# Kernel tuning notes

Measured on AMD Instinct MI355X. Metric: run time of the kernel, lower is better.

Reference implementation:

```python
import jax, jax.numpy as jnp
import numpy as np

DIM = 1024
H = 16
HD = 64

def setup_inputs() -> dict:
    key = jax.random.key(0)
    ks = jax.random.split(key, 5)
    x = jax.random.normal(ks[0], (2, 2048, DIM), dtype=jnp.float32)
    gamma = jnp.ones((DIM,), jnp.float32)
    beta = jnp.zeros((DIM,), jnp.float32)
    w_qkv = jax.random.normal(ks[1], (DIM, 3 * H * HD), dtype=jnp.float32) * (DIM ** -0.5)
    w_out = jax.random.normal(ks[2], (H * HD, DIM), dtype=jnp.float32) * ((H * HD) ** -0.5)
    b_out = jnp.zeros((DIM,), jnp.float32)
    return {"x": x, "gamma": gamma, "beta": beta, "w_qkv": w_qkv, "w_out": w_out, "b_out": b_out}

def reference(x, gamma, beta, w_qkv, w_out, b_out):
    # LayerNorm (pre-norm)
    mu = jnp.mean(x, axis=-1, keepdims=True)
    var = jnp.var(x, axis=-1, keepdims=True)
    xn = (x - mu) * jax.lax.rsqrt(var + 1e-5) * gamma + beta
    # QKV projection (no bias)
    qkv = xn @ w_qkv  # (b, n, 3*h*hd)
    q, k, v = jnp.split(qkv, 3, axis=-1)
    b, n, _ = x.shape
    split = lambda t: t.reshape(b, n, H, HD).transpose(0, 2, 1, 3)  # b h n d
    q, k, v = split(q), split(k), split(v)
    scale = HD ** -0.5
    scores = jnp.einsum('bhqd,bhkd->bhqk', q, k) * scale
    weights = jax.nn.softmax(scores, axis=-1)
    attn = jnp.einsum('bhqk,bhkd->bhqd', weights, v)  # b h n d
    attn = attn.transpose(0, 2, 1, 3).reshape(b, n, H * HD)
    # output projection (dropout is identity in eval)
    return attn @ w_out + b_out
```

## Files before the change

kernel.cpp:

```cpp
#include <hip/hip_runtime.h>
#include <hip/hip_bf16.h>


typedef _Float16 f16x8 __attribute__((ext_vector_type(8)));
typedef _Float16 f16x4 __attribute__((ext_vector_type(4)));
typedef float    f32x4 __attribute__((ext_vector_type(4)));

#define DIM   1024
#define NH    16
#define HD2   64
#define SEQ   2048
#define ROWS  4096
#define QKVN  3072
#define NT    32

__device__ __forceinline__ void async_copy16(void* lds, const void* gsrc) {
    __builtin_amdgcn_global_load_lds(
        (const __attribute__((address_space(1))) unsigned int*)gsrc,
        (__attribute__((address_space(3))) unsigned int*)lds, 16, 0, 0);
}

__global__ __launch_bounds__(256) void prologue_kernel(
    const float* __restrict__ x, const float* __restrict__ gamma,
    const float* __restrict__ beta, _Float16* __restrict__ xn,
    const float* __restrict__ w_qkv, _Float16* __restrict__ wqkvT,
    const float* __restrict__ w_out, _Float16* __restrict__ woutT) {
    __shared__ float smem[32 * 33];
    const int bid = blockIdx.x;
    const int t = threadIdx.x;
    if (bid < ROWS) {
        const int row = bid;
        const float4 v = reinterpret_cast<const float4*>(x + (size_t)row * DIM)[t];
        float s1 = v.x + v.y + v.z + v.w;
        float s2 = v.x * v.x + v.y * v.y + v.z * v.z + v.w * v.w;
        for (int off = 32; off; off >>= 1) {
            s1 += __shfl_down(s1, off);
            s2 += __shfl_down(s2, off);
        }
        const int wv = t >> 6, lane = t & 63;
        if (lane == 0) { smem[wv * 2] = s1; smem[wv * 2 + 1] = s2; }
        __syncthreads();
        s1 = smem[0] + smem[2] + smem[4] + smem[6];
        s2 = smem[1] + smem[3] + smem[5] + smem[7];
        const float mu = s1 * (1.0f / DIM);
        const float var = s2 * (1.0f / DIM) - mu * mu;
        const float rstd = rsqrtf(var + 1e-5f);
        const float4 g = reinterpret_cast<const float4*>(gamma)[t];
        const float4 bb = reinterpret_cast<const float4*>(beta)[t];
        f16x4 o;
        o[0] = (_Float16)((v.x - mu) * rstd * g.x + bb.x);
        o[1] = (_Float16)((v.y - mu) * rstd * g.y + bb.y);
        o[2] = (_Float16)((v.z - mu) * rstd * g.z + bb.z);
        o[3] = (_Float16)((v.w - mu) * rstd * g.w + bb.w);
        reinterpret_cast<f16x4*>(xn + (size_t)row * DIM)[t] = o;
        return;
    }
    const float* in;
    _Float16* out;
    int C, bx, by;
    if (bid < ROWS + (QKVN / 32) * (DIM / 32)) {
        const int q = bid - ROWS;
        in = w_qkv; out = wqkvT; C = QKVN;
        bx = q % (QKVN / 32); by = q / (QKVN / 32);
    } else {
        const int q = bid - ROWS - (QKVN / 32) * (DIM / 32);
        in = w_out; out = woutT; C = DIM;
        bx = q % (DIM / 32); by = q / (DIM / 32);
    }
    const int R = DIM;
    const int c0 = bx * 32, r0 = by * 32;
    const int tx = t & 31, ty = t >> 5;
    float (*tile)[33] = reinterpret_cast<float(*)[33]>(smem);
#pragma unroll
    for (int i = 0; i < 4; i++)
        tile[ty + i * 8][tx] = in[(size_t)(r0 + ty + i * 8) * C + c0 + tx];
    __syncthreads();
#pragma unroll
    for (int i = 0; i < 4; i++)
        out[(size_t)(c0 + ty + i * 8) * R + r0 + tx] = (_Float16)tile[tx][ty + i * 8];
}

__global__ __launch_bounds__(256) void gemm_qkv_kernel(
    const _Float16* __restrict__ A, const _Float16* __restrict__ Bt,
    _Float16* __restrict__ qk, _Float16* __restrict__ vT) {
    const int K = DIM;
    __shared__ _Float16 Al[3][128 * 32];
    __shared__ _Float16 Bl[3][128 * 32];
    const int t = threadIdx.x, wv = t >> 6, lane = t & 63;
    const int lg = lane >> 4, lr = lane & 15;
    const int wr = wv >> 1, wc = wv & 1;
    const int m0 = blockIdx.y * 128, n0 = blockIdx.x * 128;

    f32x4 acc[4][4] = {};

    const int srow = t >> 2, sk = (t & 3) * 8;
    const _Float16* Ag0 = A + (size_t)(m0 + srow) * K + sk;
    const _Float16* Bg0 = Bt + (size_t)(n0 + srow) * K + sk;

    auto STAGE = [&](int buf, int k0) {
        _Float16* Alw = &Al[buf][wv * 512];
        _Float16* Blw = &Bl[buf][wv * 512];
        async_copy16(Alw,        Ag0 + k0);
        async_copy16(Alw + 2048, Ag0 + (size_t)64 * K + k0);
        async_copy16(Blw,        Bg0 + k0);
        async_copy16(Blw + 2048, Bg0 + (size_t)64 * K + k0);
    };

    STAGE(0, 0);
    STAGE(1, 32);
    int cur = 0;
    for (int tt = 0; tt < NT; ++tt) {
        if (tt < NT - 1) asm volatile("s_waitcnt vmcnt(4)" ::: "memory");
        else             asm volatile("s_waitcnt vmcnt(0)" ::: "memory");
        __builtin_amdgcn_s_barrier();
        if (tt + 2 < NT) {
            const int wb = cur >= 1 ? cur - 1 : 2;
            STAGE(wb, (tt + 2) * 32);
        }
        const _Float16* Ab = &Al[cur][0];
        const _Float16* Bb = &Bl[cur][0];
        f16x8 af[4], bfr[4];
#pragma unroll
        for (int m = 0; m < 4; m++)
            af[m] = *reinterpret_cast<const f16x8*>(&Ab[(wr * 64 + m * 16 + lr) * 32 + lg * 8]);
#pragma unroll
        for (int n = 0; n < 4; n++)
            bfr[n] = *reinterpret_cast<const f16x8*>(&Bb[(wc * 64 + n * 16 + lr) * 32 + lg * 8]);
#pragma unroll
        for (int m = 0; m < 4; m++)
#pragma unroll
            for (int n = 0; n < 4; n++)
                acc[m][n] = __builtin_amdgcn_mfma_f32_16x16x32_f16(af[m], bfr[n], acc[m][n], 0, 0, 0);
        asm volatile("s_waitcnt lgkmcnt(0)" ::: "memory");
        cur = cur < 2 ? cur + 1 : 0;
    }

    if (n0 < 2 * DIM) {
#pragma unroll
        for (int m = 0; m < 4; m++) {
            const int row = m0 + wr * 64 + m * 16 + lg * 4;
#pragma unroll
            for (int n = 0; n < 4; n++) {
                const int col = n0 + wc * 64 + n * 16 + lr;
#pragma unroll
                for (int jj = 0; jj < 4; jj++)
                    qk[(size_t)(row + jj) * 2048 + col] = (_Float16)acc[m][n][jj];
            }
        }
    } else {
#pragma unroll
        for (int m = 0; m < 4; m++) {
            const int row = m0 + wr * 64 + m * 16 + lg * 4;
            const int b = row >> 11, nn = row & 2047;
#pragma unroll
            for (int n = 0; n < 4; n++) {
                const int vcol = n0 + wc * 64 + n * 16 + lr - 2 * DIM;
                f16x4 pk;
#pragma unroll
                for (int jj = 0; jj < 4; jj++) pk[jj] = (_Float16)acc[m][n][jj];
                *reinterpret_cast<f16x4*>(&vT[(size_t)(b * 1024 + vcol) * SEQ + nn]) = pk;
            }
        }
    }
}

__global__ __launch_bounds__(256) void gemm_out_kernel(
    const _Float16* __restrict__ A, const _Float16* __restrict__ Bt,
    float* __restrict__ C, const float* __restrict__ bias) {
    const int K = DIM, N = DIM;
    __shared__ _Float16 Al[3][128 * 32];
    __shared__ _Float16 Bl[3][64 * 32];
    const int t = threadIdx.x, wv = t >> 6, lane = t & 63;
    const int lg = lane >> 4, lr = lane & 15;
    const int wr = wv >> 1, wc = wv & 1;
    const int m0 = blockIdx.y * 128, n0 = blockIdx.x * 64;

    f32x4 acc[4][2] = {};

    const int srow = t >> 2, sk = (t & 3) * 8;
    const _Float16* Ag0 = A + (size_t)(m0 + srow) * K + sk;
    const _Float16* Bg0 = Bt + (size_t)(n0 + srow) * K + sk;

    auto STAGE = [&](int buf, int k0) {
        _Float16* Alw = &Al[buf][wv * 512];
        _Float16* Blw = &Bl[buf][wv * 512];
        async_copy16(Alw,        Ag0 + k0);
        async_copy16(Alw + 2048, Ag0 + (size_t)64 * K + k0);
        async_copy16(Blw,        Bg0 + k0);
    };

    STAGE(0, 0);
    STAGE(1, 32);
    int cur = 0;
    for (int tt = 0; tt < NT; ++tt) {
        if (tt < NT - 1) asm volatile("s_waitcnt vmcnt(3)" ::: "memory");
        else             asm volatile("s_waitcnt vmcnt(0)" ::: "memory");
        __builtin_amdgcn_s_barrier();
        if (tt + 2 < NT) {
            const int wb = cur >= 1 ? cur - 1 : 2;
            STAGE(wb, (tt + 2) * 32);
        }
        const _Float16* Ab = &Al[cur][0];
        const _Float16* Bb = &Bl[cur][0];
        f16x8 af[4], bfr[2];
#pragma unroll
        for (int m = 0; m < 4; m++)
            af[m] = *reinterpret_cast<const f16x8*>(&Ab[(wr * 64 + m * 16 + lr) * 32 + lg * 8]);
#pragma unroll
        for (int n = 0; n < 2; n++)
            bfr[n] = *reinterpret_cast<const f16x8*>(&Bb[(wc * 32 + n * 16 + lr) * 32 + lg * 8]);
#pragma unroll
        for (int m = 0; m < 4; m++)
#pragma unroll
            for (int n = 0; n < 2; n++)
                acc[m][n] = __builtin_amdgcn_mfma_f32_16x16x32_f16(af[m], bfr[n], acc[m][n], 0, 0, 0);
        asm volatile("s_waitcnt lgkmcnt(0)" ::: "memory");
        cur = cur < 2 ? cur + 1 : 0;
    }

#pragma unroll
    for (int m = 0; m < 4; m++) {
        const int row = m0 + wr * 64 + m * 16 + lg * 4;
#pragma unroll
        for (int n = 0; n < 2; n++) {
            const int col = n0 + wc * 32 + n * 16 + lr;
            const float bo = bias[col];
#pragma unroll
            for (int jj = 0; jj < 4; jj++)
                C[(size_t)(row + jj) * N + col] = acc[m][n][jj] + bo;
        }
    }
}

__global__ __launch_bounds__(256) void attn_fa_kernel(
    const _Float16* __restrict__ qk, const _Float16* __restrict__ vT,
    _Float16* __restrict__ attn) {
    const int id = blockIdx.x;
    const int nid = (id & 7) * 128 + (id >> 3);
    const int bh = nid >> 5, b = bh >> 4, h = bh & 15;
    const int q0 = (nid & 31) * 64;
    const int t = threadIdx.x, wv = t >> 6, lane = t & 63;
    const int lg = lane >> 4, lr = lane & 15;

    __shared__ _Float16 Kl[64][72];
    __shared__ _Float16 Vt[64][72];
    __shared__ _Float16 PT[4][16][72];

    const size_t qrow = (size_t)(b * SEQ + q0 + wv * 16 + lr);
    const _Float16* qp = qk + qrow * 2048 + h * HD2;
    f16x8 qf0 = *reinterpret_cast<const f16x8*>(qp + lg * 8);
    f16x8 qf1 = *reinterpret_cast<const f16x8*>(qp + 32 + lg * 8);
    qf0 = qf0 * (_Float16)0.125f;
    qf1 = qf1 * (_Float16)0.125f;

    f32x4 o[4] = {};
    float mrun = -INFINITY, lrun = 0.f;

    const int sr = t >> 3, sc = (t & 7) * 8;
    const _Float16* kbase = qk + (size_t)(b * SEQ + sr) * 2048 + DIM + h * HD2 + sc;
    const _Float16* vbase = vT + (size_t)(bh * HD2 + sr) * SEQ + sc;

    f16x8 rk0 = *reinterpret_cast<const f16x8*>(kbase);
    f16x8 rk1 = *reinterpret_cast<const f16x8*>(kbase + (size_t)32 * 2048);
    f16x8 rv0 = *reinterpret_cast<const f16x8*>(vbase);
    f16x8 rv1 = *reinterpret_cast<const f16x8*>(vbase + (size_t)32 * SEQ);

    for (int kv0 = 0; kv0 < SEQ; kv0 += 64) {
        __builtin_amdgcn_s_barrier();
        *reinterpret_cast<f16x8*>(&Kl[sr][sc])      = rk0;
        *reinterpret_cast<f16x8*>(&Kl[sr + 32][sc]) = rk1;
        *reinterpret_cast<f16x8*>(&Vt[sr][sc])      = rv0;
        *reinterpret_cast<f16x8*>(&Vt[sr + 32][sc]) = rv1;
        if (kv0 + 64 < SEQ) {
            const _Float16* kp = kbase + (size_t)(kv0 + 64) * 2048;
            const _Float16* vp = vbase + (kv0 + 64);
            rk0 = *reinterpret_cast<const f16x8*>(kp);
            rk1 = *reinterpret_cast<const f16x8*>(kp + (size_t)32 * 2048);
            rv0 = *reinterpret_cast<const f16x8*>(vp);
            rv1 = *reinterpret_cast<const f16x8*>(vp + (size_t)32 * SEQ);
        }
        asm volatile("s_waitcnt lgkmcnt(0)" ::: "memory");
        __builtin_amdgcn_s_barrier();

        f32x4 s[4];
#pragma unroll
        for (int n = 0; n < 4; n++) {
            f16x8 kf0 = *reinterpret_cast<const f16x8*>(&Kl[n * 16 + lr][lg * 8]);
            f16x8 kf1 = *reinterpret_cast<const f16x8*>(&Kl[n * 16 + lr][32 + lg * 8]);
            f32x4 z = {0.f, 0.f, 0.f, 0.f};
            __builtin_amdgcn_s_setprio(1);
            z = __builtin_amdgcn_mfma_f32_16x16x32_f16(kf0, qf0, z, 0, 0, 0);
            z = __builtin_amdgcn_mfma_f32_16x16x32_f16(kf1, qf1, z, 0, 0, 0);
            __builtin_amdgcn_s_setprio(0);
            s[n] = z;
        }

        float m1 = fmaxf(fmaxf(s[0][0], s[0][1]), fmaxf(s[0][2], s[0][3]));
#pragma unroll
        for (int n = 1; n < 4; n++)
            m1 = fmaxf(m1, fmaxf(fmaxf(s[n][0], s[n][1]), fmaxf(s[n][2], s[n][3])));
        m1 = fmaxf(m1, __shfl_xor(m1, 16));
        m1 = fmaxf(m1, __shfl_xor(m1, 32));
        if (!__all(m1 - mrun <= 8.f)) {
            const float mnew = fmaxf(mrun, m1);
            const float corr = __expf(mrun - mnew);
            mrun = mnew;
            lrun *= corr;
#pragma unroll
            for (int dn = 0; dn < 4; dn++) o[dn] *= corr;
        }
        float rsum = 0.f;
#pragma unroll
        for (int n = 0; n < 4; n++)
#pragma unroll
            for (int jj = 0; jj < 4; jj++) {
                const float p = __expf(s[n][jj] - mrun);
                s[n][jj] = p;
                rsum += p;
            }
        rsum += __shfl_xor(rsum, 16);
        rsum += __shfl_xor(rsum, 32);
        lrun += rsum;

#pragma unroll
        for (int n = 0; n < 4; n++) {
            f16x4 pk;
#pragma unroll
            for (int jj = 0; jj < 4; jj++) pk[jj] = (_Float16)s[n][jj];
            *reinterpret_cast<f16x4*>(&PT[wv][lr][n * 16 + lg * 4]) = pk;
        }
        f16x8 pa0 = *reinterpret_cast<const f16x8*>(&PT[wv][lr][lg * 8]);
        f16x8 pa1 = *reinterpret_cast<const f16x8*>(&PT[wv][lr][32 + lg * 8]);

#pragma unroll
        for (int dn = 0; dn < 4; dn++) {
            f16x8 vf0 = *reinterpret_cast<const f16x8*>(&Vt[dn * 16 + lr][lg * 8]);
            f16x8 vf1 = *reinterpret_cast<const f16x8*>(&Vt[dn * 16 + lr][32 + lg * 8]);
            __builtin_amdgcn_s_setprio(1);
            o[dn] = __builtin_amdgcn_mfma_f32_16x16x32_f16(vf0, pa0, o[dn], 0, 0, 0);
            o[dn] = __builtin_amdgcn_mfma_f32_16x16x32_f16(vf1, pa1, o[dn], 0, 0, 0);
            __builtin_amdgcn_s_setprio(0);
        }
    }

    const float inv = 1.0f / lrun;
    const size_t orow = (size_t)(b * SEQ + q0 + wv * 16 + lr);
#pragma unroll
    for (int dn = 0; dn < 4; dn++) {
        f16x4 pk;
#pragma unroll
        for (int jj = 0; jj < 4; jj++) pk[jj] = (_Float16)(o[dn][jj] * inv);
        *reinterpret_cast<f16x4*>(&attn[orow * DIM + h * HD2 + dn * 16 + lg * 4]) = pk;
    }
}

extern "C" void kernel_launch(void* const* d_in, const int* in_sizes, int n_in,
                              void* d_out, int out_size, void* d_ws, size_t ws_size,
                              hipStream_t stream) {
    const float* x     = (const float*)d_in[0];
    const float* gamma = (const float*)d_in[1];
    const float* beta  = (const float*)d_in[2];
    const float* w_qkv = (const float*)d_in[3];
    const float* w_out = (const float*)d_in[4];
    const float* b_out = (const float*)d_in[5];
    float* out = (float*)d_out;

    _Float16* ws    = (_Float16*)d_ws;
    _Float16* xn    = ws;
    _Float16* wqkvT = xn + (size_t)ROWS * DIM;
    _Float16* woutT = wqkvT + (size_t)QKVN * DIM;
    _Float16* qk    = woutT + (size_t)DIM * DIM;
    _Float16* vT    = qk + (size_t)ROWS * 2048;
    _Float16* attnb = xn;

    const int pro_blocks = ROWS + (QKVN / 32) * (DIM / 32) + (DIM / 32) * (DIM / 32);
    prologue_kernel<<<pro_blocks, 256, 0, stream>>>(x, gamma, beta, xn, w_qkv, wqkvT, w_out, woutT);
    gemm_qkv_kernel<<<dim3(QKVN / 128, ROWS / 128), 256, 0, stream>>>(xn, wqkvT, qk, vT);
    attn_fa_kernel<<<1024, 256, 0, stream>>>(qk, vT, attnb);
    gemm_out_kernel<<<dim3(DIM / 64, ROWS / 128), 256, 0, stream>>>(attnb, woutT, out, b_out);
}
```

Baseline: 220.7 us.

## Rework attention to 128-query tiles with double-buffered K/V and register P

The attention kernel now processes 128 queries per block, two 16-row query slices per wave, so each K/V tile staged in LDS is reused twice. K/V tiles are double-buffered in LDS with a single barrier per iteration, and P is repacked in registers instead of going through an LDS round trip. The GEMM kernels drop from triple to double buffering with a runtime K and a full barrier per step. In exchange, the attention grid halves to 512 blocks and uses more registers (launch bounds 2), and the GEMM pipeline is shallower and may hide less latency.

```diff
diff --git a/kernel.cpp b/kernel.cpp
--- a/kernel.cpp
+++ b/kernel.cpp
@@ -12,7 +12,6 @@
 #define SEQ   2048
 #define ROWS  4096
 #define QKVN  3072
-#define NT    32
 
 __device__ __forceinline__ void async_copy16(void* lds, const void* gsrc) {
     __builtin_amdgcn_global_load_lds(
@@ -82,10 +81,9 @@
 
 __global__ __launch_bounds__(256) void gemm_qkv_kernel(
     const _Float16* __restrict__ A, const _Float16* __restrict__ Bt,
-    _Float16* __restrict__ qk, _Float16* __restrict__ vT) {
-    const int K = DIM;
-    __shared__ _Float16 Al[3][128 * 32];
-    __shared__ _Float16 Bl[3][128 * 32];
+    _Float16* __restrict__ qk, _Float16* __restrict__ vT, int K) {
+    __shared__ _Float16 Al[2][128 * 32];
+    __shared__ _Float16 Bl[2][128 * 32];
     const int t = threadIdx.x, wv = t >> 6, lane = t & 63;
     const int lg = lane >> 4, lr = lane & 15;
     const int wr = wv >> 1, wc = wv & 1;
@@ -107,16 +105,11 @@
     };
 
     STAGE(0, 0);
-    STAGE(1, 32);
+    asm volatile("s_waitcnt vmcnt(0)" ::: "memory");
+    __builtin_amdgcn_s_barrier();
     int cur = 0;
-    for (int tt = 0; tt < NT; ++tt) {
-        if (tt < NT - 1) asm volatile("s_waitcnt vmcnt(4)" ::: "memory");
-        else             asm volatile("s_waitcnt vmcnt(0)" ::: "memory");
-        __builtin_amdgcn_s_barrier();
-        if (tt + 2 < NT) {
-            const int wb = cur >= 1 ? cur - 1 : 2;
-            STAGE(wb, (tt + 2) * 32);
-        }
+    for (int k0 = 0; k0 < K; k0 += 32) {
+        if (k0 + 32 < K) STAGE(cur ^ 1, k0 + 32);
         const _Float16* Ab = &Al[cur][0];
         const _Float16* Bb = &Bl[cur][0];
         f16x8 af[4], bfr[4];
@@ -131,8 +124,9 @@
 #pragma unroll
             for (int n = 0; n < 4; n++)
                 acc[m][n] = __builtin_amdgcn_mfma_f32_16x16x32_f16(af[m], bfr[n], acc[m][n], 0, 0, 0);
-        asm volatile("s_waitcnt lgkmcnt(0)" ::: "memory");
-        cur = cur < 2 ? cur + 1 : 0;
+        asm volatile("s_waitcnt vmcnt(0)" ::: "memory");
+        __builtin_amdgcn_s_barrier();
+        cur ^= 1;
     }
 
     if (n0 < 2 * DIM) {
@@ -166,10 +160,9 @@
 
 __global__ __launch_bounds__(256) void gemm_out_kernel(
     const _Float16* __restrict__ A, const _Float16* __restrict__ Bt,
-    float* __restrict__ C, const float* __restrict__ bias) {
-    const int K = DIM, N = DIM;
-    __shared__ _Float16 Al[3][128 * 32];
-    __shared__ _Float16 Bl[3][64 * 32];
+    float* __restrict__ C, const float* __restrict__ bias, int N, int K) {
+    __shared__ _Float16 Al[2][128 * 32];
+    __shared__ _Float16 Bl[2][64 * 32];
     const int t = threadIdx.x, wv = t >> 6, lane = t & 63;
     const int lg = lane >> 4, lr = lane & 15;
     const int wr = wv >> 1, wc = wv & 1;
@@ -190,16 +183,11 @@
     };
 
     STAGE(0, 0);
-    STAGE(1, 32);
+    asm volatile("s_waitcnt vmcnt(0)" ::: "memory");
+    __builtin_amdgcn_s_barrier();
     int cur = 0;
-    for (int tt = 0; tt < NT; ++tt) {
-        if (tt < NT - 1) asm volatile("s_waitcnt vmcnt(3)" ::: "memory");
-        else             asm volatile("s_waitcnt vmcnt(0)" ::: "memory");
-        __builtin_amdgcn_s_barrier();
-        if (tt + 2 < NT) {
-            const int wb = cur >= 1 ? cur - 1 : 2;
-            STAGE(wb, (tt + 2) * 32);
-        }
+    for (int k0 = 0; k0 < K; k0 += 32) {
+        if (k0 + 32 < K) STAGE(cur ^ 1, k0 + 32);
         const _Float16* Ab = &Al[cur][0];
         const _Float16* Bb = &Bl[cur][0];
         f16x8 af[4], bfr[2];
@@ -214,8 +202,9 @@
 #pragma unroll
             for (int n = 0; n < 2; n++)
                 acc[m][n] = __builtin_amdgcn_mfma_f32_16x16x32_f16(af[m], bfr[n], acc[m][n], 0, 0, 0);
-        asm volatile("s_waitcnt lgkmcnt(0)" ::: "memory");
-        cur = cur < 2 ? cur + 1 : 0;
+        asm volatile("s_waitcnt vmcnt(0)" ::: "memory");
+        __builtin_amdgcn_s_barrier();
+        cur ^= 1;
     }
 
 #pragma unroll
@@ -232,29 +221,33 @@
     }
 }
 
-__global__ __launch_bounds__(256) void attn_fa_kernel(
+__global__ __launch_bounds__(256, 2) void attn_fa_kernel(
     const _Float16* __restrict__ qk, const _Float16* __restrict__ vT,
     _Float16* __restrict__ attn) {
     const int id = blockIdx.x;
-    const int nid = (id & 7) * 128 + (id >> 3);
-    const int bh = nid >> 5, b = bh >> 4, h = bh & 15;
-    const int q0 = (nid & 31) * 64;
+    const int nid = (id & 7) * 64 + (id >> 3);
+    const int bh = nid >> 4, b = bh >> 4, h = bh & 15;
+    const int q0 = (nid & 15) * 128;
     const int t = threadIdx.x, wv = t >> 6, lane = t & 63;
     const int lg = lane >> 4, lr = lane & 15;
 
-    __shared__ _Float16 Kl[64][72];
-    __shared__ _Float16 Vt[64][72];
-    __shared__ _Float16 PT[4][16][72];
-
-    const size_t qrow = (size_t)(b * SEQ + q0 + wv * 16 + lr);
-    const _Float16* qp = qk + qrow * 2048 + h * HD2;
-    f16x8 qf0 = *reinterpret_cast<const f16x8*>(qp + lg * 8);
-    f16x8 qf1 = *reinterpret_cast<const f16x8*>(qp + 32 + lg * 8);
-    qf0 = qf0 * (_Float16)0.125f;
-    qf1 = qf1 * (_Float16)0.125f;
-
-    f32x4 o[4] = {};
-    float mrun = -INFINITY, lrun = 0.f;
+    __shared__ _Float16 Kl[2][64][72];
+    __shared__ _Float16 Vt[2][64][72];
+
+    const _Float16* qb = qk + (size_t)(b * SEQ + q0 + wv * 32 + lr) * 2048 + h * HD2;
+    f16x8 qf[2][2];
+    qf[0][0] = *reinterpret_cast<const f16x8*>(qb + lg * 8);
+    qf[0][1] = *reinterpret_cast<const f16x8*>(qb + 32 + lg * 8);
+    qf[1][0] = *reinterpret_cast<const f16x8*>(qb + (size_t)16 * 2048 + lg * 8);
+    qf[1][1] = *reinterpret_cast<const f16x8*>(qb + (size_t)16 * 2048 + 32 + lg * 8);
+#pragma unroll
+    for (int qs = 0; qs < 2; qs++) {
+        qf[qs][0] = qf[qs][0] * (_Float16)0.125f;
+        qf[qs][1] = qf[qs][1] * (_Float16)0.125f;
+    }
+
+    f32x4 o[2][4] = {};
+    float mrun[2] = {-INFINITY, -INFINITY}, lrun[2] = {0.f, 0.f};
 
     const int sr = t >> 3, sc = (t & 7) * 8;
     const _Float16* kbase = qk + (size_t)(b * SEQ + sr) * 2048 + DIM + h * HD2 + sc;
@@ -264,93 +257,127 @@
     f16x8 rk1 = *reinterpret_cast<const f16x8*>(kbase + (size_t)32 * 2048);
     f16x8 rv0 = *reinterpret_cast<const f16x8*>(vbase);
     f16x8 rv1 = *reinterpret_cast<const f16x8*>(vbase + (size_t)32 * SEQ);
-
-    for (int kv0 = 0; kv0 < SEQ; kv0 += 64) {
-        __builtin_amdgcn_s_barrier();
-        *reinterpret_cast<f16x8*>(&Kl[sr][sc])      = rk0;
-        *reinterpret_cast<f16x8*>(&Kl[sr + 32][sc]) = rk1;
-        *reinterpret_cast<f16x8*>(&Vt[sr][sc])      = rv0;
-        *reinterpret_cast<f16x8*>(&Vt[sr + 32][sc]) = rv1;
+    *reinterpret_cast<f16x8*>(&Kl[0][sr][sc])      = rk0;
+    *reinterpret_cast<f16x8*>(&Kl[0][sr + 32][sc]) = rk1;
+    *reinterpret_cast<f16x8*>(&Vt[0][sr][sc])      = rv0;
+    *reinterpret_cast<f16x8*>(&Vt[0][sr + 32][sc]) = rv1;
+    rk0 = *reinterpret_cast<const f16x8*>(kbase + (size_t)64 * 2048);
+    rk1 = *reinterpret_cast<const f16x8*>(kbase + (size_t)96 * 2048);
+    rv0 = *reinterpret_cast<const f16x8*>(vbase + 64);
+    rv1 = *reinterpret_cast<const f16x8*>(vbase + (size_t)32 * SEQ + 64);
+    asm volatile("s_waitcnt lgkmcnt(0)" ::: "memory");
+    __builtin_amdgcn_s_barrier();
+
+    int p = 0;
+    for (int kv0 = 0; kv0 < SEQ; kv0 += 64, p ^= 1) {
         if (kv0 + 64 < SEQ) {
-            const _Float16* kp = kbase + (size_t)(kv0 + 64) * 2048;
-            const _Float16* vp = vbase + (kv0 + 64);
-            rk0 = *reinterpret_cast<const f16x8*>(kp);
-            rk1 = *reinterpret_cast<const f16x8*>(kp + (size_t)32 * 2048);
-            rv0 = *reinterpret_cast<const f16x8*>(vp);
-            rv1 = *reinterpret_cast<const f16x8*>(vp + (size_t)32 * SEQ);
+            *reinterpret_cast<f16x8*>(&Kl[p ^ 1][sr][sc])      = rk0;
+            *reinterpret_cast<f16x8*>(&Kl[p ^ 1][sr + 32][sc]) = rk1;
+            *reinterpret_cast<f16x8*>(&Vt[p ^ 1][sr][sc])      = rv0;
+            *reinterpret_cast<f16x8*>(&Vt[p ^ 1][sr + 32][sc]) = rv1;
+            if (kv0 + 128 < SEQ) {
+                const _Float16* kp = kbase + (size_t)(kv0 + 128) * 2048;
+                const _Float16* vp = vbase + (kv0 + 128);
+                rk0 = *reinterpret_cast<const f16x8*>(kp);
+                rk1 = *reinterpret_cast<const f16x8*>(kp + (size_t)32 * 2048);
+                rv0 = *reinterpret_cast<const f16x8*>(vp);
+                rv1 = *reinterpret_cast<const f16x8*>(vp + (size_t)32 * SEQ);
+            }
+        }
+
+        f32x4 s[2][4];
+#pragma unroll
+        for (int n = 0; n < 4; n++) {
+            f16x8 kf0 = *reinterpret_cast<const f16x8*>(&Kl[p][n * 16 + lr][lg * 8]);
+            f16x8 kf1 = *reinterpret_cast<const f16x8*>(&Kl[p][n * 16 + lr][32 + lg * 8]);
+            __builtin_amdgcn_s_setprio(1);
+#pragma unroll
+            for (int qs = 0; qs < 2; qs++) {
+                f32x4 z = {0.f, 0.f, 0.f, 0.f};
+                z = __builtin_amdgcn_mfma_f32_16x16x32_f16(kf0, qf[qs][0], z, 0, 0, 0);
+                z = __builtin_amdgcn_mfma_f32_16x16x32_f16(kf1, qf[qs][1], z, 0, 0, 0);
+                s[qs][n] = z;
+            }
+            __builtin_amdgcn_s_setprio(0);
+        }
+
+        f16x8 pa[2][2];
+#pragma unroll
+        for (int qs = 0; qs < 2; qs++) {
+            float m1 = fmaxf(fmaxf(s[qs][0][0], s[qs][0][1]), fmaxf(s[qs][0][2], s[qs][0][3]));
+#pragma unroll
+            for (int n = 1; n < 4; n++)
+                m1 = fmaxf(m1, fmaxf(fmaxf(s[qs][n][0], s[qs][n][1]), fmaxf(s[qs][n][2], s[qs][n][3])));
+            m1 = fmaxf(m1, __shfl_xor(m1, 16));
+            m1 = fmaxf(m1, __shfl_xor(m1, 32));
+            if (!__all(m1 - mrun[qs] <= 8.f)) {
+                const float mnew = fmaxf(mrun[qs], m1);
+                const float corr = __expf(mrun[qs] - mnew);
+                mrun[qs] = mnew;
+                lrun[qs] *= corr;
+#pragma unroll
+                for (int dn = 0; dn < 4; dn++) o[qs][dn] *= corr;
+            }
+            float rsum = 0.f;
+#pragma unroll
+            for (int n = 0; n < 4; n++)
+#pragma unroll
+                for (int jj = 0; jj < 4; jj++) {
+                    const float pv = __expf(s[qs][n][jj] - mrun[qs]);
+                    s[qs][n][jj] = pv;
+                    rsum += pv;
+                }
+            rsum += __shfl_xor(rsum, 16);
+            rsum += __shfl_xor(rsum, 32);
+            lrun[qs] += rsum;
+#pragma unroll
+            for (int m = 0; m < 2; m++) {
+                f16x8 pv;
+#pragma unroll
+                for (int jj = 0; jj < 4; jj++) {
+                    pv[jj]     = (_Float16)s[qs][2 * m][jj];
+                    pv[4 + jj] = (_Float16)s[qs][2 * m + 1][jj];
+                }
+                pa[qs][m] = pv;
+            }
+        }
+
+#pragma unroll
+        for (int dn = 0; dn < 4; dn++) {
+            const _Float16* vr = &Vt[p][dn * 16 + lr][0];
+            f16x4 va0 = *reinterpret_cast<const f16x4*>(vr + lg * 4);
+            f16x4 va1 = *reinterpret_cast<const f16x4*>(vr + 16 + lg * 4);
+            f16x4 vb0 = *reinterpret_cast<const f16x4*>(vr + 32 + lg * 4);
+            f16x4 vb1 = *reinterpret_cast<const f16x4*>(vr + 48 + lg * 4);
+            f16x8 vf0, vf1;
+#pragma unroll
+            for (int j = 0; j < 4; j++) {
+                vf0[j] = va0[j]; vf0[4 + j] = va1[j];
+                vf1[j] = vb0[j]; vf1[4 + j] = vb1[j];
+            }
+            __builtin_amdgcn_s_setprio(1);
+#pragma unroll
+            for (int qs = 0; qs < 2; qs++) {
+                o[qs][dn] = __builtin_amdgcn_mfma_f32_16x16x32_f16(vf0, pa[qs][0], o[qs][dn], 0, 0, 0);
+                o[qs][dn] = __builtin_amdgcn_mfma_f32_16x16x32_f16(vf1, pa[qs][1], o[qs][dn], 0, 0, 0);
+            }
+            __builtin_amdgcn_s_setprio(0);
         }
         asm volatile("s_waitcnt lgkmcnt(0)" ::: "memory");
         __builtin_amdgcn_s_barrier();
-
-        f32x4 s[4];
-#pragma unroll
-        for (int n = 0; n < 4; n++) {
-            f16x8 kf0 = *reinterpret_cast<const f16x8*>(&Kl[n * 16 + lr][lg * 8]);
-            f16x8 kf1 = *reinterpret_cast<const f16x8*>(&Kl[n * 16 + lr][32 + lg * 8]);
-            f32x4 z = {0.f, 0.f, 0.f, 0.f};
-            __builtin_amdgcn_s_setprio(1);
-            z = __builtin_amdgcn_mfma_f32_16x16x32_f16(kf0, qf0, z, 0, 0, 0);
-            z = __builtin_amdgcn_mfma_f32_16x16x32_f16(kf1, qf1, z, 0, 0, 0);
-            __builtin_amdgcn_s_setprio(0);
-            s[n] = z;
-        }
-
-        float m1 = fmaxf(fmaxf(s[0][0], s[0][1]), fmaxf(s[0][2], s[0][3]));
-#pragma unroll
-        for (int n = 1; n < 4; n++)
-            m1 = fmaxf(m1, fmaxf(fmaxf(s[n][0], s[n][1]), fmaxf(s[n][2], s[n][3])));
-        m1 = fmaxf(m1, __shfl_xor(m1, 16));
-        m1 = fmaxf(m1, __shfl_xor(m1, 32));
-        if (!__all(m1 - mrun <= 8.f)) {
-            const float mnew = fmaxf(mrun, m1);
-            const float corr = __expf(mrun - mnew);
-            mrun = mnew;
-            lrun *= corr;
-#pragma unroll
-            for (int dn = 0; dn < 4; dn++) o[dn] *= corr;
-        }
-        float rsum = 0.f;
-#pragma unroll
-        for (int n = 0; n < 4; n++)
-#pragma unroll
-            for (int jj = 0; jj < 4; jj++) {
-                const float p = __expf(s[n][jj] - mrun);
-                s[n][jj] = p;
-                rsum += p;
-            }
-        rsum += __shfl_xor(rsum, 16);
-        rsum += __shfl_xor(rsum, 32);
-        lrun += rsum;
-
-#pragma unroll
-        for (int n = 0; n < 4; n++) {
+    }
+
+#pragma unroll
+    for (int qs = 0; qs < 2; qs++) {
+        const float inv = 1.0f / lrun[qs];
+        const size_t orow = (size_t)(b * SEQ + q0 + wv * 32 + qs * 16 + lr);
+#pragma unroll
+        for (int dn = 0; dn < 4; dn++) {
             f16x4 pk;
 #pragma unroll
-            for (int jj = 0; jj < 4; jj++) pk[jj] = (_Float16)s[n][jj];
-            *reinterpret_cast<f16x4*>(&PT[wv][lr][n * 16 + lg * 4]) = pk;
-        }
-        f16x8 pa0 = *reinterpret_cast<const f16x8*>(&PT[wv][lr][lg * 8]);
-        f16x8 pa1 = *reinterpret_cast<const f16x8*>(&PT[wv][lr][32 + lg * 8]);
-
-#pragma unroll
-        for (int dn = 0; dn < 4; dn++) {
-            f16x8 vf0 = *reinterpret_cast<const f16x8*>(&Vt[dn * 16 + lr][lg * 8]);
-            f16x8 vf1 = *reinterpret_cast<const f16x8*>(&Vt[dn * 16 + lr][32 + lg * 8]);
-            __builtin_amdgcn_s_setprio(1);
-            o[dn] = __builtin_amdgcn_mfma_f32_16x16x32_f16(vf0, pa0, o[dn], 0, 0, 0);
-            o[dn] = __builtin_amdgcn_mfma_f32_16x16x32_f16(vf1, pa1, o[dn], 0, 0, 0);
-            __builtin_amdgcn_s_setprio(0);
-        }
-    }
-
-    const float inv = 1.0f / lrun;
-    const size_t orow = (size_t)(b * SEQ + q0 + wv * 16 + lr);
-#pragma unroll
-    for (int dn = 0; dn < 4; dn++) {
-        f16x4 pk;
-#pragma unroll
-        for (int jj = 0; jj < 4; jj++) pk[jj] = (_Float16)(o[dn][jj] * inv);
-        *reinterpret_cast<f16x4*>(&attn[orow * DIM + h * HD2 + dn * 16 + lg * 4]) = pk;
+            for (int jj = 0; jj < 4; jj++) pk[jj] = (_Float16)(o[qs][dn][jj] * inv);
+            *reinterpret_cast<f16x4*>(&attn[orow * DIM + h * HD2 + dn * 16 + lg * 4]) = pk;
+        }
     }
 }
 
@@ -375,7 +402,7 @@
 
     const int pro_blocks = ROWS + (QKVN / 32) * (DIM / 32) + (DIM / 32) * (DIM / 32);
     prologue_kernel<<<pro_blocks, 256, 0, stream>>>(x, gamma, beta, xn, w_qkv, wqkvT, w_out, woutT);
-    gemm_qkv_kernel<<<dim3(QKVN / 128, ROWS / 128), 256, 0, stream>>>(xn, wqkvT, qk, vT);
-    attn_fa_kernel<<<1024, 256, 0, stream>>>(qk, vT, attnb);
-    gemm_out_kernel<<<dim3(DIM / 64, ROWS / 128), 256, 0, stream>>>(attnb, woutT, out, b_out);
-}
+    gemm_qkv_kernel<<<dim3(QKVN / 128, ROWS / 128), 256, 0, stream>>>(xn, wqkvT, qk, vT, DIM);
+    attn_fa_kernel<<<512, 256, 0, stream>>>(qk, vT, attnb);
+    gemm_out_kernel<<<dim3(DIM / 64, ROWS / 128), 256, 0, stream>>>(attnb, woutT, out, b_out, DIM, DIM);
+}
```

Result: faster. 205.4 us (-6.9%).
